# Performance work log

Measured on AMD Instinct MI355X. Metric: run time of the kernel, lower is better.

The kernel has to match this reference:

```python
import jax, jax.numpy as jnp
import numpy as np

ENC_DIM, DEC_DIM, JOINT_DIM, VOCAB = 512, 640, 512, 1024
B, T, U = 8, 256, 64


def setup_inputs() -> dict:
    key = jax.random.key(0)
    ks = jax.random.split(key, 8)
    s_enc = 1.0 / np.sqrt(ENC_DIM)
    s_dec = 1.0 / np.sqrt(DEC_DIM)
    s_out = 1.0 / np.sqrt(2 * JOINT_DIM)
    return {
        "enc_out": jax.random.normal(ks[0], (B, T, ENC_DIM), jnp.float32),
        "pred_out": jax.random.normal(ks[1], (B, U, DEC_DIM), jnp.float32),
        "W_enc": jax.random.uniform(ks[2], (JOINT_DIM, ENC_DIM), jnp.float32, -s_enc, s_enc),
        "b_enc": jax.random.uniform(ks[3], (JOINT_DIM,), jnp.float32, -s_enc, s_enc),
        "W_pred": jax.random.uniform(ks[4], (JOINT_DIM, DEC_DIM), jnp.float32, -s_dec, s_dec),
        "b_pred": jax.random.uniform(ks[5], (JOINT_DIM,), jnp.float32, -s_dec, s_dec),
        "W_out": jax.random.uniform(ks[6], (VOCAB, 2 * JOINT_DIM), jnp.float32, -s_out, s_out),
        "b_out": jax.random.uniform(ks[7], (VOCAB,), jnp.float32, -s_out, s_out),
    }


def reference(enc_out, pred_out, W_enc, b_enc, W_pred, b_pred, W_out, b_out):
    # Dropout is identity in eval mode. fc_out on cat([enc_exp, pred_exp]) is
    # mathematically identical to splitting W_out in half and summing two
    # broadcast projections (avoids materializing the [B,T,U,2J] tensor).
    J = W_enc.shape[0]
    e = jnp.einsum('bte,je->btj', enc_out, W_enc) + b_enc    # [B,T,J]
    p = jnp.einsum('bud,jd->buj', pred_out, W_pred) + b_pred  # [B,U,J]
    W1, W2 = W_out[:, :J], W_out[:, J:]
    out = (jnp.einsum('btj,vj->btv', e, W1)[:, :, None, :]
           + jnp.einsum('buj,vj->buv', p, W2)[:, None, :, :]
           + b_out)                                           # [B,T,U,V]
    return out
```

## Files before the change

### kernel.cpp

```cpp
#include <hip/hip_runtime.h>

typedef float f4 __attribute__((ext_vector_type(4)));
typedef float f32x4 __attribute__((ext_vector_type(4)));
typedef short bf16x8 __attribute__((ext_vector_type(8)));
typedef unsigned short u16x8 __attribute__((ext_vector_type(8)));

static __device__ __forceinline__ unsigned short f2bf(float f) {
    unsigned int x = __builtin_bit_cast(unsigned int, f);
    x = (x + 0x7fffu + ((x >> 16) & 1u)) >> 16;
    return (unsigned short)x;
}
static __device__ __forceinline__ float bf2f(unsigned short h) {
    unsigned int x = ((unsigned int)h) << 16;
    return __builtin_bit_cast(float, x);
}

static __device__ __forceinline__ void gll16(const unsigned short* g, unsigned short* l) {
    __builtin_amdgcn_global_load_lds(
        (__attribute__((address_space(1))) void*)(g),
        (__attribute__((address_space(3))) void*)(l), 16, 0, 0);
}

static __device__ __forceinline__ int fragoff(int r, int s) {
    return r * 32 + ((s ^ ((r >> 1) & 3)) << 3);
}

struct GJobF {
    const float *A, *W;
    int lda, ldw;
    const float* bias;
    unsigned short *Ch, *Cl;
    int N, K, nbx;
};

__global__ __launch_bounds__(256, 3) void gemmcvt64(
    GJobF j0, GJobF j1, int nblk0, int nblk1,
    const float* __restrict__ Wo, unsigned short* __restrict__ Wo_h, int nWo8)
{
    __shared__ unsigned short lds[2][3][64 * 32];

    const int bid = blockIdx.x;
    const int tid = threadIdx.x;

    if (bid >= nblk0 + nblk1) {
        const int nblkc = (int)gridDim.x - nblk0 - nblk1;
        for (int g = (bid - nblk0 - nblk1) * 256 + tid; g < nWo8; g += nblkc * 256) {
            const int idx = g * 8;
            f4 a = *(const f4*)(Wo + idx);
            f4 b = *(const f4*)(Wo + idx + 4);
            u16x8 hv;
            float s[8] = { a.x, a.y, a.z, a.w, b.x, b.y, b.z, b.w };
            #pragma unroll
            for (int i = 0; i < 8; ++i) hv[i] = f2bf(s[i]);
            *(u16x8*)(Wo_h + idx) = hv;
        }
        return;
    }

    const bool first = bid < nblk0;
    const GJobF J = first ? j0 : j1;
    const int local = first ? bid : bid - nblk0;
    const int m0 = (local % J.nbx) * 64;
    const int n0 = (local / J.nbx) * 64;

    const int lane = tid & 63;
    const int wid  = tid >> 6;
    const int wr   = wid >> 1, wc = wid & 1;
    const int lrow = lane & 15;
    const int s    = lane >> 4;

    const int row  = tid >> 2, slot = tid & 3;
    const int woff = fragoff(row, slot);
    const float* pA = J.A + (size_t)(m0 + row) * J.lda + slot * 8;
    const float* pW = J.W + (size_t)(n0 + row) * J.ldw + slot * 8;

    f4 ra0, ra1, rw0, rw1;

#define LOADREGS(k0) do { \
    ra0 = *(const f4*)(pA + (k0));     ra1 = *(const f4*)(pA + (k0) + 4); \
    rw0 = *(const f4*)(pW + (k0));     rw1 = *(const f4*)(pW + (k0) + 4); \
} while (0)

#define CVTWRITE(buf) do { \
    u16x8 ha, la, hw; \
    float sa[8] = { ra0.x, ra0.y, ra0.z, ra0.w, ra1.x, ra1.y, ra1.z, ra1.w }; \
    float sw[8] = { rw0.x, rw0.y, rw0.z, rw0.w, rw1.x, rw1.y, rw1.z, rw1.w }; \
    _Pragma("unroll") \
    for (int i = 0; i < 8; ++i) { \
        unsigned short h = f2bf(sa[i]); \
        ha[i] = h; la[i] = f2bf(sa[i] - bf2f(h)); \
        hw[i] = f2bf(sw[i]); \
    } \
    *(u16x8*)&lds[buf][0][woff] = ha; \
    *(u16x8*)&lds[buf][1][woff] = la; \
    *(u16x8*)&lds[buf][2][woff] = hw; \
} while (0)

    f32x4 acc[2][2];
    #pragma unroll
    for (int i = 0; i < 2; ++i)
        #pragma unroll
        for (int j = 0; j < 2; ++j) acc[i][j] = (f32x4){0.f, 0.f, 0.f, 0.f};

    const int nt = J.K / 32;

    LOADREGS(0);
    CVTWRITE(0);
    __syncthreads();

    int cur = 0;
    for (int t = 0; t < nt; ++t) {
        if (t + 1 < nt) LOADREGS((t + 1) * 32);

        bf16x8 ah[2], al[2], wh[2];
        #pragma unroll
        for (int i = 0; i < 2; ++i) {
            const int ra = wr * 32 + i * 16 + lrow;
            const int rw = wc * 32 + i * 16 + lrow;
            ah[i] = *(const bf16x8*)&lds[cur][0][fragoff(ra, s)];
            al[i] = *(const bf16x8*)&lds[cur][1][fragoff(ra, s)];
            wh[i] = *(const bf16x8*)&lds[cur][2][fragoff(rw, s)];
        }
        #pragma unroll
        for (int i = 0; i < 2; ++i)
            #pragma unroll
            for (int j = 0; j < 2; ++j) {
                acc[i][j] = __builtin_amdgcn_mfma_f32_16x16x32_bf16(ah[i], wh[j], acc[i][j], 0, 0, 0);
                acc[i][j] = __builtin_amdgcn_mfma_f32_16x16x32_bf16(al[i], wh[j], acc[i][j], 0, 0, 0);
            }

        if (t + 1 < nt) {
            CVTWRITE(cur ^ 1);
            __syncthreads();
            cur ^= 1;
        }
    }
#undef LOADREGS
#undef CVTWRITE

    #pragma unroll
    for (int i = 0; i < 2; ++i) {
        const int rbase = m0 + wr * 32 + i * 16 + (lane >> 4) * 4;
        #pragma unroll
        for (int j = 0; j < 2; ++j) {
            const int col = n0 + wc * 32 + j * 16 + (lane & 15);
            const float bv = J.bias[col];
            #pragma unroll
            for (int r = 0; r < 4; ++r) {
                float v = acc[i][j][r] + bv;
                size_t off = (size_t)(rbase + r) * J.N + col;
                unsigned short h = f2bf(v);
                J.Ch[off] = h;
                J.Cl[off] = f2bf(v - bf2f(h));
            }
        }
    }
}

struct GJob {
    const unsigned short *Ah, *Al, *Wh;
    int lda, ldw;
    const float* bias;
    float* Cf;
    int N, K, nbx;
};

__global__ __launch_bounds__(256, 4) void gemm64x128(GJob j0, GJob j1, int nblk0)
{
    __shared__ unsigned short lds[2][4][64 * 32];

    const bool first = (int)blockIdx.x < nblk0;
    const GJob J = first ? j0 : j1;
    const int local = first ? (int)blockIdx.x : (int)blockIdx.x - nblk0;
    const int m0 = (local % J.nbx) * 64;
    const int n0 = (local / J.nbx) * 128;

    const int tid  = threadIdx.x;
    const int lane = tid & 63;
    const int wid  = tid >> 6;
    const int wr   = wid >> 1, wc = wid & 1;
    const int lrow = lane & 15;
    const int s    = lane >> 4;

    const int arow  = wid * 16 + (lane >> 2);
    const int aslot = (lane & 3) ^ ((arow >> 1) & 3);
    const size_t gA = (size_t)(m0 + arow) * J.lda + aslot * 8;
    const int wrow0 = wid * 32 + (lane >> 2);
    const int wrow1 = wrow0 + 16;
    const int wsl0  = (lane & 3) ^ ((wrow0 >> 1) & 3);
    const int wsl1  = (lane & 3) ^ ((wrow1 >> 1) & 3);
    const size_t gW0 = (size_t)(n0 + wrow0) * J.ldw + wsl0 * 8;
    const size_t gW1 = (size_t)(n0 + wrow1) * J.ldw + wsl1 * 8;

#define STAGE(buf, k0) do { \
    gll16(J.Ah + gA + (k0),  &lds[buf][0][wid * 512]); \
    gll16(J.Al + gA + (k0),  &lds[buf][1][wid * 512]); \
    gll16(J.Wh + gW0 + (k0), &lds[buf][2 + (wid >> 1)][(wid & 1) * 1024]); \
    gll16(J.Wh + gW1 + (k0), &lds[buf][2 + (wid >> 1)][(wid & 1) * 1024 + 512]); \
} while (0)

    f32x4 acc[2][4];
    #pragma unroll
    for (int i = 0; i < 2; ++i)
        #pragma unroll
        for (int j = 0; j < 4; ++j) acc[i][j] = (f32x4){0.f, 0.f, 0.f, 0.f};

    const int nt = J.K / 32;

    STAGE(0, 0);
    asm volatile("s_waitcnt vmcnt(0)" ::: "memory");
    __syncthreads();

    int cur = 0;
    for (int t = 0; t < nt; ++t) {
        if (t + 1 < nt) STAGE(cur ^ 1, (t + 1) * 32);

        bf16x8 ah[2], al[2], wh[4];
        #pragma unroll
        for (int i = 0; i < 2; ++i) {
            const int ra = wr * 32 + i * 16 + lrow;
            ah[i] = *(const bf16x8*)&lds[cur][0][fragoff(ra, s)];
            al[i] = *(const bf16x8*)&lds[cur][1][fragoff(ra, s)];
        }
        #pragma unroll
        for (int j = 0; j < 4; ++j) {
            const int rw = wc * 64 + j * 16 + lrow;
            wh[j] = *(const bf16x8*)&lds[cur][2 + (rw >> 6)][fragoff(rw & 63, s)];
        }
        #pragma unroll
        for (int i = 0; i < 2; ++i)
            #pragma unroll
            for (int j = 0; j < 4; ++j) {
                acc[i][j] = __builtin_amdgcn_mfma_f32_16x16x32_bf16(ah[i], wh[j], acc[i][j], 0, 0, 0);
                acc[i][j] = __builtin_amdgcn_mfma_f32_16x16x32_bf16(al[i], wh[j], acc[i][j], 0, 0, 0);
            }

        if (t + 1 < nt) {
            asm volatile("s_waitcnt vmcnt(0)" ::: "memory");
            __syncthreads();
            cur ^= 1;
        }
    }
#undef STAGE

    #pragma unroll
    for (int i = 0; i < 2; ++i) {
        const int rbase = m0 + wr * 32 + i * 16 + (lane >> 4) * 4;
        #pragma unroll
        for (int j = 0; j < 4; ++j) {
            const int col = n0 + wc * 64 + j * 16 + (lane & 15);
            const float bv = J.bias ? J.bias[col] : 0.f;
            #pragma unroll
            for (int r = 0; r < 4; ++r)
                J.Cf[(size_t)(rbase + r) * J.N + col] = acc[i][j][r] + bv;
        }
    }
}

__global__ __launch_bounds__(256) void bcast_kernel(
    const float* __restrict__ X, const float* __restrict__ Y,
    float* __restrict__ out, int T, int U)
{
    const int Vq  = 256;
    const int bt  = blockIdx.x;
    const int b   = bt / T;
    const int tid = threadIdx.x;

    const f4* X4 = (const f4*)X;
    const f4* Y4 = (const f4*)Y + (size_t)b * U * Vq;
    f4* O4 = (f4*)out + (size_t)bt * U * Vq;

    f4 x = X4[(size_t)bt * Vq + tid];
    #pragma unroll 4
    for (int u = 0; u < U; ++u) {
        f4 y = Y4[u * Vq + tid];
        f4 r = { x.x + y.x, x.y + y.y, x.z + y.z, x.w + y.w };
        __builtin_nontemporal_store(r, &O4[u * Vq + tid]);
    }
}

extern "C" void kernel_launch(void* const* d_in, const int* in_sizes, int n_in,
                              void* d_out, int out_size, void* d_ws, size_t ws_size,
                              hipStream_t stream) {
    (void)in_sizes; (void)n_in; (void)out_size; (void)ws_size;

    const int B = 8, T = 256, U = 64;
    const int ENC = 512, DEC = 640, J = 512, V = 1024;
    const int MT = B * T;
    const int MU = B * U;

    const float* enc    = (const float*)d_in[0];
    const float* pred   = (const float*)d_in[1];
    const float* W_enc  = (const float*)d_in[2];
    const float* b_enc  = (const float*)d_in[3];
    const float* W_pred = (const float*)d_in[4];
    const float* b_pred = (const float*)d_in[5];
    const float* W_out  = (const float*)d_in[6];
    const float* b_out  = (const float*)d_in[7];
    float* out = (float*)d_out;

    const int n_Wo = V * 2 * J;
    const int n_e  = MT * J;
    const int n_p  = MU * J;

    unsigned short* w = (unsigned short*)d_ws;
    unsigned short* Wo_h = w;
    unsigned short* e_h  = Wo_h + n_Wo;
    unsigned short* e_l  = e_h + n_e;
    unsigned short* p_h  = e_l + n_e;
    unsigned short* p_l  = p_h + n_p;
    float* ws_X = (float*)(p_l + n_p);
    float* ws_Y = ws_X + (size_t)MT * V;

    GJobF je = { enc,  W_enc,  ENC, ENC, b_enc,  e_h, e_l, J, ENC, MT / 64 };
    GJobF jp = { pred, W_pred, DEC, DEC, b_pred, p_h, p_l, J, DEC, MU / 64 };
    const int nbe = (MT / 64) * (J / 64);
    const int nbp = (MU / 64) * (J / 64);
    const int ncv = 64;
    gemmcvt64<<<nbe + nbp + ncv, 256, 0, stream>>>(
        je, jp, nbe, nbp, W_out, Wo_h, n_Wo / 8);

    GJob jx = { e_h, e_l, Wo_h,     J, 2 * J, b_out,   ws_X, V, J, MT / 64 };
    GJob jy = { p_h, p_l, Wo_h + J, J, 2 * J, nullptr, ws_Y, V, J, MU / 64 };
    const int nbx = (MT / 64) * (V / 128);
    const int nby = (MU / 64) * (V / 128);
    gemm64x128<<<nbx + nby, 256, 0, stream>>>(jx, jy, nbx);

    bcast_kernel<<<dim3(B * T), 256, 0, stream>>>(ws_X, ws_Y, out, T, U);
}
```

Baseline: 131.9 us.

## Fuse output GEMM and broadcast into one persistent kernel with flag-based dependencies

```diff
diff --git a/kernel.cpp b/kernel.cpp
--- a/kernel.cpp
+++ b/kernel.cpp
@@ -157,25 +157,14 @@
     }
 }
 
-struct GJob {
-    const unsigned short *Ah, *Al, *Wh;
-    int lda, ldw;
-    const float* bias;
-    float* Cf;
-    int N, K, nbx;
-};
-
-__global__ __launch_bounds__(256, 4) void gemm64x128(GJob j0, GJob j1, int nblk0)
+
+static __device__ __forceinline__ void gemm_tile_64x128(
+    unsigned short* lds,
+    const unsigned short* __restrict__ Ah, const unsigned short* __restrict__ Al,
+    const unsigned short* __restrict__ Wh, int lda, int ldw, int K,
+    const float* __restrict__ bias, float* __restrict__ Cf, int N,
+    int m0, int n0, int tid)
 {
-    __shared__ unsigned short lds[2][4][64 * 32];
-
-    const bool first = (int)blockIdx.x < nblk0;
-    const GJob J = first ? j0 : j1;
-    const int local = first ? (int)blockIdx.x : (int)blockIdx.x - nblk0;
-    const int m0 = (local % J.nbx) * 64;
-    const int n0 = (local / J.nbx) * 128;
-
-    const int tid  = threadIdx.x;
     const int lane = tid & 63;
     const int wid  = tid >> 6;
     const int wr   = wid >> 1, wc = wid & 1;
@@ -184,19 +173,19 @@
 
     const int arow  = wid * 16 + (lane >> 2);
     const int aslot = (lane & 3) ^ ((arow >> 1) & 3);
-    const size_t gA = (size_t)(m0 + arow) * J.lda + aslot * 8;
+    const size_t gA = (size_t)(m0 + arow) * lda + aslot * 8;
     const int wrow0 = wid * 32 + (lane >> 2);
     const int wrow1 = wrow0 + 16;
     const int wsl0  = (lane & 3) ^ ((wrow0 >> 1) & 3);
     const int wsl1  = (lane & 3) ^ ((wrow1 >> 1) & 3);
-    const size_t gW0 = (size_t)(n0 + wrow0) * J.ldw + wsl0 * 8;
-    const size_t gW1 = (size_t)(n0 + wrow1) * J.ldw + wsl1 * 8;
+    const size_t gW0 = (size_t)(n0 + wrow0) * ldw + wsl0 * 8;
+    const size_t gW1 = (size_t)(n0 + wrow1) * ldw + wsl1 * 8;
 
 #define STAGE(buf, k0) do { \
-    gll16(J.Ah + gA + (k0),  &lds[buf][0][wid * 512]); \
-    gll16(J.Al + gA + (k0),  &lds[buf][1][wid * 512]); \
-    gll16(J.Wh + gW0 + (k0), &lds[buf][2 + (wid >> 1)][(wid & 1) * 1024]); \
-    gll16(J.Wh + gW1 + (k0), &lds[buf][2 + (wid >> 1)][(wid & 1) * 1024 + 512]); \
+    gll16(Ah + gA + (k0),  &lds[((buf) * 4 + 0) * 2048 + wid * 512]); \
+    gll16(Al + gA + (k0),  &lds[((buf) * 4 + 1) * 2048 + wid * 512]); \
+    gll16(Wh + gW0 + (k0), &lds[((buf) * 4 + 2 + (wid >> 1)) * 2048 + (wid & 1) * 1024]); \
+    gll16(Wh + gW1 + (k0), &lds[((buf) * 4 + 2 + (wid >> 1)) * 2048 + (wid & 1) * 1024 + 512]); \
 } while (0)
 
     f32x4 acc[2][4];
@@ -205,7 +194,7 @@
         #pragma unroll
         for (int j = 0; j < 4; ++j) acc[i][j] = (f32x4){0.f, 0.f, 0.f, 0.f};
 
-    const int nt = J.K / 32;
+    const int nt = K / 32;
 
     STAGE(0, 0);
     asm volatile("s_waitcnt vmcnt(0)" ::: "memory");
@@ -219,13 +208,13 @@
         #pragma unroll
         for (int i = 0; i < 2; ++i) {
             const int ra = wr * 32 + i * 16 + lrow;
-            ah[i] = *(const bf16x8*)&lds[cur][0][fragoff(ra, s)];
-            al[i] = *(const bf16x8*)&lds[cur][1][fragoff(ra, s)];
+            ah[i] = *(const bf16x8*)&lds[(cur * 4 + 0) * 2048 + fragoff(ra, s)];
+            al[i] = *(const bf16x8*)&lds[(cur * 4 + 1) * 2048 + fragoff(ra, s)];
         }
         #pragma unroll
         for (int j = 0; j < 4; ++j) {
             const int rw = wc * 64 + j * 16 + lrow;
-            wh[j] = *(const bf16x8*)&lds[cur][2 + (rw >> 6)][fragoff(rw & 63, s)];
+            wh[j] = *(const bf16x8*)&lds[(cur * 4 + 2 + (rw >> 6)) * 2048 + fragoff(rw & 63, s)];
         }
         #pragma unroll
         for (int i = 0; i < 2; ++i)
@@ -249,33 +238,83 @@
         #pragma unroll
         for (int j = 0; j < 4; ++j) {
             const int col = n0 + wc * 64 + j * 16 + (lane & 15);
-            const float bv = J.bias ? J.bias[col] : 0.f;
+            const float bv = bias ? bias[col] : 0.f;
             #pragma unroll
             for (int r = 0; r < 4; ++r)
-                J.Cf[(size_t)(rbase + r) * J.N + col] = acc[i][j][r] + bv;
-        }
-    }
-}
-
-__global__ __launch_bounds__(256) void bcast_kernel(
-    const float* __restrict__ X, const float* __restrict__ Y,
-    float* __restrict__ out, int T, int U)
+                Cf[(size_t)(rbase + r) * N + col] = acc[i][j][r] + bv;
+        }
+    }
+    __syncthreads();
+}
+
+__global__ __launch_bounds__(128) void zero_flags(int* flags, int n) {
+    if ((int)threadIdx.x < n) flags[threadIdx.x] = 0;
+}
+
+#define NG 192
+__global__ __launch_bounds__(256, 4) void fused2(
+    const unsigned short* __restrict__ e_h, const unsigned short* __restrict__ e_l,
+    const unsigned short* __restrict__ p_h, const unsigned short* __restrict__ p_l,
+    const unsigned short* __restrict__ Wo_h,
+    const float* __restrict__ b_out,
+    float* ws_X, float* ws_Y, float* __restrict__ out, int* flags)
 {
-    const int Vq  = 256;
-    const int bt  = blockIdx.x;
-    const int b   = bt / T;
+    __shared__ unsigned short lds[2 * 4 * 2048];
+    __shared__ int s_job;
     const int tid = threadIdx.x;
 
-    const f4* X4 = (const f4*)X;
-    const f4* Y4 = (const f4*)Y + (size_t)b * U * Vq;
-    f4* O4 = (f4*)out + (size_t)bt * U * Vq;
-
-    f4 x = X4[(size_t)bt * Vq + tid];
-    #pragma unroll 4
-    for (int u = 0; u < U; ++u) {
-        f4 y = Y4[u * Vq + tid];
-        f4 r = { x.x + y.x, x.y + y.y, x.z + y.z, x.w + y.w };
-        __builtin_nontemporal_store(r, &O4[u * Vq + tid]);
+    int* job_ctr = flags + 0;
+    int* y_f = flags + 1;
+    int* x_f = flags + 2;
+
+    if ((int)blockIdx.x < NG) {
+        for (;;) {
+            __syncthreads();
+            if (tid == 0) s_job = atomicAdd(job_ctr, 1);
+            __syncthreads();
+            const int j = s_job;
+            if (j >= 320) return;
+            if (j < 64) {
+                const int m = j >> 3, n = j & 7;
+                gemm_tile_64x128(lds, p_h, p_l, Wo_h + 512, 512, 1024, 512,
+                                 nullptr, ws_Y, 1024, m * 64, n * 128, tid);
+                __syncthreads();
+                if (tid == 0)
+                    __hip_atomic_fetch_add(y_f, 1, __ATOMIC_RELEASE, __HIP_MEMORY_SCOPE_AGENT);
+            } else {
+                const int jl = j - 64, m = jl >> 3, n = jl & 7;
+                gemm_tile_64x128(lds, e_h, e_l, Wo_h, 512, 1024, 512,
+                                 b_out, ws_X, 1024, m * 64, n * 128, tid);
+                __syncthreads();
+                if (tid == 0)
+                    __hip_atomic_fetch_add(&x_f[m], 1, __ATOMIC_RELEASE, __HIP_MEMORY_SCOPE_AGENT);
+            }
+        }
+    }
+
+    const int bt0 = ((int)blockIdx.x - NG) * 4;
+    if (tid == 0) {
+        while (__hip_atomic_load(y_f, __ATOMIC_RELAXED, __HIP_MEMORY_SCOPE_AGENT) < 64)
+            __builtin_amdgcn_s_sleep(8);
+        while (__hip_atomic_load(&x_f[bt0 >> 6], __ATOMIC_RELAXED, __HIP_MEMORY_SCOPE_AGENT) < 8)
+            __builtin_amdgcn_s_sleep(8);
+        (void)__hip_atomic_load(y_f, __ATOMIC_ACQUIRE, __HIP_MEMORY_SCOPE_AGENT);
+    }
+    __syncthreads();
+
+    const int b = bt0 >> 8;
+    const f4* Y4 = (const f4*)ws_Y + (size_t)b * 64 * 256;
+    #pragma unroll
+    for (int r = 0; r < 4; ++r) {
+        const int bt = bt0 + r;
+        f4 x = ((const f4*)ws_X)[(size_t)bt * 256 + tid];
+        f4* O4 = (f4*)out + (size_t)bt * 64 * 256;
+        #pragma unroll 4
+        for (int u = 0; u < 64; ++u) {
+            f4 y = Y4[u * 256 + tid];
+            f4 v = { x.x + y.x, x.y + y.y, x.z + y.z, x.w + y.w };
+            __builtin_nontemporal_store(v, &O4[u * 256 + tid]);
+        }
     }
 }
 
@@ -311,6 +350,9 @@
     unsigned short* p_l  = p_h + n_p;
     float* ws_X = (float*)(p_l + n_p);
     float* ws_Y = ws_X + (size_t)MT * V;
+    int*   flags = (int*)(ws_Y + (size_t)MU * V);
+
+    zero_flags<<<1, 128, 0, stream>>>(flags, 34);
 
     GJobF je = { enc,  W_enc,  ENC, ENC, b_enc,  e_h, e_l, J, ENC, MT / 64 };
     GJobF jp = { pred, W_pred, DEC, DEC, b_pred, p_h, p_l, J, DEC, MU / 64 };
@@ -320,11 +362,6 @@
     gemmcvt64<<<nbe + nbp + ncv, 256, 0, stream>>>(
         je, jp, nbe, nbp, W_out, Wo_h, n_Wo / 8);
 
-    GJob jx = { e_h, e_l, Wo_h,     J, 2 * J, b_out,   ws_X, V, J, MT / 64 };
-    GJob jy = { p_h, p_l, Wo_h + J, J, 2 * J, nullptr, ws_Y, V, J, MU / 64 };
-    const int nbx = (MT / 64) * (V / 128);
-    const int nby = (MU / 64) * (V / 128);
-    gemm64x128<<<nbx + nby, 256, 0, stream>>>(jx, jy, nbx);
-
-    bcast_kernel<<<dim3(B * T), 256, 0, stream>>>(ws_X, ws_Y, out, T, U);
-}
+    fused2<<<NG + 512, 256, 0, stream>>>(
+        e_h, e_l, p_h, p_l, Wo_h, b_out, ws_X, ws_Y, out, flags);
+}
```

Result: slower. 179.7 us (+36.2%).
